# Performance work log

Hardware: AMD Instinct MI355X
Metric: run time of the kernel (lower is better)

Reference implementation:

```python
import jax, jax.numpy as jnp
import numpy as np

NG, ND, NS, E, DIM, H = 20000, 8000, 8000, 300000, 256, 8
HD = DIM // H
SCALE = 1.0 / float(np.sqrt(HD))
EPS = 1e-5


def _ln(x, g, b):
    mu = x.mean(-1, keepdims=True)
    var = ((x - mu) ** 2).mean(-1, keepdims=True)
    return (x - mu) / jnp.sqrt(var + EPS) * g + b


def _attn(h_src, h_dst, Wq, bq, Wk, bk, Wv, bv, src, dst, n_dst):
    # multi-head edge dot-product attention with edge_softmax over incoming edges
    Q = (h_dst @ Wq.T + bq).reshape(-1, H, HD)
    K = (h_src @ Wk.T + bk).reshape(-1, H, HD)
    V = (h_src @ Wv.T + bv).reshape(-1, H, HD)
    score = jnp.einsum('ehd,ehd->eh', K[src], Q[dst]) * SCALE  # [E, H]
    m = jax.ops.segment_max(score, dst, num_segments=n_dst)
    m = jnp.where(jnp.isfinite(m), m, 0.0)  # nodes with no in-edges
    a = jnp.exp(score - m[dst])
    denom = jax.ops.segment_sum(a, dst, num_segments=n_dst)
    a = a / denom[dst]
    h = jax.ops.segment_sum(V[src] * a[:, :, None], dst, num_segments=n_dst)
    return h.reshape(n_dst, DIM)


def _bahdanau(m1, m2, W1, b1, W2, b2, v, bv):
    e1 = (jnp.tanh(m1 @ W1.T + b1) @ v.T + bv)[:, 0]
    e2 = (jnp.tanh(m2 @ W2.T + b2) @ v.T + bv)[:, 0]
    w = jax.nn.softmax(jnp.stack([e1, e2], axis=1), axis=1)
    return w[:, 0:1] * m1 + w[:, 1:2] * m2


def _forward(gene_feat, drug_feat, disease_feat,
             dg_Wq, dg_bq, dg_Wk, dg_bk, dg_Wv, dg_bv,
             disg_Wq, disg_bq, disg_Wk, disg_bk, disg_Wv, disg_bv,
             gd_Wq, gd_bq, gd_Wk, gd_bk, gd_Wv, gd_bv,
             gdis_Wq, gdis_bq, gdis_Wk, gdis_bk, gdis_Wv, gdis_bv,
             f_W1, f_b1, f_W2, f_b2, f_v, f_bv,
             ln1_g, ln1_b, ln2_g, ln2_b,
             dg_src, dg_dst, disg_src, disg_dst, gd_src, gd_dst, gdis_src, gdis_dst):
    gm_drug = _attn(drug_feat, gene_feat, dg_Wq, dg_bq, dg_Wk, dg_bk, dg_Wv, dg_bv, dg_src, dg_dst, NG)
    gm_dis = _attn(disease_feat, gene_feat, disg_Wq, disg_bq, disg_Wk, disg_bk, disg_Wv, disg_bv, disg_src, disg_dst, NG)
    has_d = jnp.zeros((NG,), bool).at[dg_dst].set(True)
    has_s = jnp.zeros((NG,), bool).at[disg_dst].set(True)
    fused = _bahdanau(gm_drug, gm_dis, f_W1, f_b1, f_W2, f_b2, f_v, f_bv)
    gene_msg = jnp.where((has_d & has_s)[:, None], fused,
                         jnp.where(has_d[:, None], gm_drug,
                                   jnp.where(has_s[:, None], gm_dis, 0.0)))
    gene_out = _ln(gene_feat + jax.nn.gelu(gene_msg, approximate=False), ln1_g, ln1_b)
    drug_msg = _attn(gene_out, drug_feat, gd_Wq, gd_bq, gd_Wk, gd_bk, gd_Wv, gd_bv, gd_src, gd_dst, ND)
    dis_msg = _attn(gene_out, disease_feat, gdis_Wq, gdis_bq, gdis_Wk, gdis_bk, gdis_Wv, gdis_bv, gdis_src, gdis_dst, NS)
    drug_out = _ln(drug_feat + jax.nn.gelu(drug_msg, approximate=False), ln2_g, ln2_b)
    disease_out = _ln(disease_feat + jax.nn.gelu(dis_msg, approximate=False), ln2_g, ln2_b)
    return (drug_out, disease_out, gene_out)


def setup_inputs() -> dict:
    ks = jax.random.split(jax.random.key(0), 40)
    it = iter(range(40))

    def nrm(shape):
        return jax.random.normal(ks[next(it)], shape, dtype=jnp.float32)

    def xav(din, dout):
        lim = float(np.sqrt(6.0 / (din + dout)))
        return jax.random.uniform(ks[next(it)], (dout, din), minval=-lim, maxval=lim, dtype=jnp.float32)

    def ridx(n, hi):
        return jax.random.randint(ks[next(it)], (n,), 0, hi, dtype=jnp.int32)

    inp = {}
    inp['gene_feat'] = nrm((NG, DIM))
    inp['drug_feat'] = nrm((ND, DIM))
    inp['disease_feat'] = nrm((NS, DIM))
    for p in ['dg', 'disg', 'gd', 'gdis']:
        inp[p + '_Wq'] = xav(DIM, DIM)
        inp[p + '_bq'] = jnp.zeros((DIM,), jnp.float32)
        inp[p + '_Wk'] = xav(DIM, DIM)
        inp[p + '_bk'] = jnp.zeros((DIM,), jnp.float32)
        inp[p + '_Wv'] = xav(DIM, DIM)
        inp[p + '_bv'] = jnp.zeros((DIM,), jnp.float32)
    inp['f_W1'] = xav(DIM, DIM); inp['f_b1'] = jnp.zeros((DIM,), jnp.float32)
    inp['f_W2'] = xav(DIM, DIM); inp['f_b2'] = jnp.zeros((DIM,), jnp.float32)
    inp['f_v'] = xav(DIM, 1); inp['f_bv'] = jnp.zeros((1,), jnp.float32)
    inp['ln1_g'] = jnp.ones((DIM,), jnp.float32); inp['ln1_b'] = jnp.zeros((DIM,), jnp.float32)
    inp['ln2_g'] = jnp.ones((DIM,), jnp.float32); inp['ln2_b'] = jnp.zeros((DIM,), jnp.float32)
    inp['dg_src'] = ridx(E, ND); inp['dg_dst'] = ridx(E, NG)
    inp['disg_src'] = ridx(E, NS); inp['disg_dst'] = ridx(E, NG)
    inp['gd_src'] = ridx(E, NG); inp['gd_dst'] = ridx(E, ND)
    inp['gdis_src'] = ridx(E, NG); inp['gdis_dst'] = ridx(E, NS)
    return inp


def reference(gene_feat, drug_feat, disease_feat,
              dg_Wq, dg_bq, dg_Wk, dg_bk, dg_Wv, dg_bv,
              disg_Wq, disg_bq, disg_Wk, disg_bk, disg_Wv, disg_bv,
              gd_Wq, gd_bq, gd_Wk, gd_bk, gd_Wv, gd_bv,
              gdis_Wq, gdis_bq, gdis_Wk, gdis_bk, gdis_Wv, gdis_bv,
              f_W1, f_b1, f_W2, f_b2, f_v, f_bv,
              ln1_g, ln1_b, ln2_g, ln2_b,
              dg_src, dg_dst, disg_src, disg_dst, gd_src, gd_dst, gdis_src, gdis_dst):
    return _forward(gene_feat, drug_feat, disease_feat,
                    dg_Wq, dg_bq, dg_Wk, dg_bk, dg_Wv, dg_bv,
                    disg_Wq, disg_bq, disg_Wk, disg_bk, disg_Wv, disg_bv,
                    gd_Wq, gd_bq, gd_Wk, gd_bk, gd_Wv, gd_bv,
                    gdis_Wq, gdis_bq, gdis_Wk, gdis_bk, gdis_Wv, gdis_bv,
                    f_W1, f_b1, f_W2, f_b2, f_v, f_bv,
                    ln1_g, ln1_b, ln2_g, ln2_b,
                    dg_src, dg_dst, disg_src, disg_dst, gd_src, gd_dst, gdis_src, gdis_dst)
```

## Files before the change

### kernel.cpp

```cpp
#include <hip/hip_runtime.h>

#define NG 20000
#define ND 8000
#define NS 8000
#define EE 300000
#define DIM 256
#define SCALE_QK 0.17677669529663687f
#define LNEPS 1e-5f

#define MAXB 40
#define L1CH 2048
#define NCH1 ((EE + L1CH - 1) / L1CH)
#define CB_G 8704
#define CB_S 10496
#define RB_G (40 * CB_G)
#define RB_S (32 * CB_S)

typedef __attribute__((ext_vector_type(4))) float floatx4;
typedef __attribute__((ext_vector_type(8))) short shortx8;
typedef __attribute__((ext_vector_type(8))) unsigned short ushortx8;
typedef unsigned int u32;

__device__ __forceinline__ float bf2f(unsigned short u) {
    union { unsigned u; float f; } c; c.u = ((unsigned)u) << 16; return c.f;
}
__device__ __forceinline__ unsigned short f2bf(float f) {
    union { float f; unsigned u; } c; c.f = f;
    return (unsigned short)((c.u + 0x7fffu + ((c.u >> 16) & 1u)) >> 16);
}
__device__ __forceinline__ float gelu_exact(float v) {
    return 0.5f * v * (1.0f + erff(v * 0.70710678118654752f));
}

__device__ __forceinline__ void async_load16(const unsigned short* g,
                                             unsigned short* lds) {
    __builtin_amdgcn_global_load_lds(
        (const __attribute__((address_space(1))) u32*)(const void*)g,
        (__attribute__((address_space(3))) u32*)(void*)lds, 16, 0, 0);
}

__device__ __forceinline__ int swzoff(int row, int q) {
    int p = (row >> 1) & 7, b = row & 1;
    return ((row >> 4) * 64 + p * 8 + (((b << 2) + q) ^ p)) * 8;
}

template <int MODE, int KVI>
__global__ __launch_bounds__(256, 4) void gemm_nt(
    const unsigned short* __restrict__ A, const unsigned short* __restrict__ W,
    const float* __restrict__ bias1, const float* __restrict__ bias2,
    const float* __restrict__ bias3, const float* __restrict__ bias4,
    unsigned short* __restrict__ C, int ldc,
    const float* __restrict__ vvec, float* __restrict__ evec, int M)
{
    __shared__ unsigned short As[2][128 * 32];
    __shared__ unsigned short Bs[2][64 * 32];
    const int tid = threadIdx.x;
    const int lane = tid & 63, wv = tid >> 6;
    const int quad = lane >> 4, l16 = lane & 15;
    const int m0 = blockIdx.x * 128;
    const int n0 = blockIdx.y * 64;

    const int sp = lane >> 3, ss = lane & 7;
    const int srow = 2 * sp + ((ss ^ sp) >> 2);
    const int sq = (ss ^ sp) & 3;
    const unsigned short* gA0 = A + (size_t)(m0 + wv * 16 + srow) * 256 + sq * 8;
    const unsigned short* gA1 = A + (size_t)(m0 + 64 + wv * 16 + srow) * 256 + sq * 8;
    const unsigned short* gB  = W + (size_t)(n0 + wv * 16 + srow) * 256 + sq * 8;

    floatx4 acc[2][4];
#pragma unroll
    for (int i = 0; i < 2; ++i)
#pragma unroll
        for (int j = 0; j < 4; ++j) acc[i][j] = (floatx4){0.f, 0.f, 0.f, 0.f};

    async_load16(gA0, &As[0][(wv * 16) * 32]);
    async_load16(gA1, &As[0][(64 + wv * 16) * 32]);
    async_load16(gB,  &Bs[0][(wv * 16) * 32]);
    __syncthreads();

    for (int k0 = 0; k0 < 256; k0 += 32) {
        const int buf = (k0 >> 5) & 1;
        if (k0 < 224) {
            const int nb = buf ^ 1;
            async_load16(gA0 + k0 + 32, &As[nb][(wv * 16) * 32]);
            async_load16(gA1 + k0 + 32, &As[nb][(64 + wv * 16) * 32]);
            async_load16(gB + k0 + 32,  &Bs[nb][(wv * 16) * 32]);
        }
        shortx8 af[2], bfr[4];
#pragma unroll
        for (int mf = 0; mf < 2; ++mf)
            af[mf] = *(const shortx8*)(&As[buf][swzoff(wv * 32 + mf * 16 + l16, quad)]);
#pragma unroll
        for (int nf = 0; nf < 4; ++nf)
            bfr[nf] = *(const shortx8*)(&Bs[buf][swzoff(nf * 16 + l16, quad)]);
#pragma unroll
        for (int mf = 0; mf < 2; ++mf)
#pragma unroll
            for (int nf = 0; nf < 4; ++nf)
                acc[mf][nf] = __builtin_amdgcn_mfma_f32_16x16x32_bf16(
                    af[mf], bfr[nf], acc[mf][nf], 0, 0, 0);
        __syncthreads();
    }

    if (MODE == 0) {
#pragma unroll
        for (int mf = 0; mf < 2; ++mf)
#pragma unroll
            for (int r = 0; r < 4; ++r) {
                int m = m0 + wv * 32 + mf * 16 + quad * 4 + r;
                if (m < M) {
#pragma unroll
                    for (int nf = 0; nf < 4; ++nf) {
                        int n = n0 + nf * 16 + l16;
                        int h = n >> 8;
                        const float* bp = (h == 0) ? bias1 : (h == 1) ? bias2
                                        : (h == 2) ? bias3 : bias4;
                        float bn = bp[n & 255];
                        int pos;
                        if (KVI) {
                            int nn = n & 511;
                            pos = (n & ~511) + ((nn & 255) >> 2) * 8 + (nn & 3) +
                                  ((nn >> 8) << 2);
                        } else {
                            pos = n;
                        }
                        C[(size_t)m * ldc + pos] = f2bf(acc[mf][nf][r] + bn);
                    }
                }
            }
    } else {
        float p[2][4] = {};
#pragma unroll
        for (int mf = 0; mf < 2; ++mf)
#pragma unroll
            for (int nf = 0; nf < 4; ++nf) {
                int n = n0 + nf * 16 + l16;
                float vn = vvec[n];
                float bn = bias1[n];
#pragma unroll
                for (int r = 0; r < 4; ++r)
                    p[mf][r] += vn * tanhf(acc[mf][nf][r] + bn);
            }
#pragma unroll
        for (int mf = 0; mf < 2; ++mf)
#pragma unroll
            for (int r = 0; r < 4; ++r) {
                float s = p[mf][r];
                s += __shfl_xor(s, 1); s += __shfl_xor(s, 2);
                s += __shfl_xor(s, 4); s += __shfl_xor(s, 8);
                if (l16 == 0) {
                    int m = m0 + wv * 32 + mf * 16 + quad * 4 + r;
                    if (m < M) atomicAdd(&evec[m], s);
                }
            }
    }
}

struct PrepP {
    int* zb; int zn; int nzb;
    const float* wsrc[14];
    unsigned short* wout;
    const float* gf; const float* df; const float* sf;
    unsigned short* go; unsigned short* dfo; unsigned short* so;
};
__global__ void prep_kernel(PrepP p) {
    int bid = blockIdx.x, tid = threadIdx.x;
    if (bid < p.nzb) {
        int i = bid * 256 + tid;
        if (i < p.zn) p.zb[i] = 0;
        return;
    }
    bid -= p.nzb;
    if (bid < 896) {
        int idx = bid * 256 + tid;
        int mat = idx >> 14;
        int e = (idx & 16383) << 2;
        float4 f = *(const float4*)(p.wsrc[mat] + e);
        ushort4 t;
        t.x = f2bf(f.x); t.y = f2bf(f.y); t.z = f2bf(f.z); t.w = f2bf(f.w);
        *(ushort4*)(p.wout + ((size_t)mat << 16) + e) = t;
        return;
    }
    bid -= 896;
    const int NG4 = NG * 64, ND4 = ND * 64, NS4 = NS * 64;
    int i = bid * 256 + tid;
    const float* in; unsigned short* out; int j;
    if (i < NG4) { in = p.gf; out = p.go; j = i; }
    else if (i < NG4 + ND4) { in = p.df; out = p.dfo; j = i - NG4; }
    else if (i < NG4 + ND4 + NS4) { in = p.sf; out = p.so; j = i - NG4 - ND4; }
    else return;
    float4 f = *(const float4*)(in + (size_t)j * 4);
    ushort4 t;
    t.x = f2bf(f.x); t.y = f2bf(f.y); t.z = f2bf(f.z); t.w = f2bf(f.w);
    *(ushort4*)(out + (size_t)j * 4) = t;
}

__global__ void fillf_kernel(float* __restrict__ p, int n, float v) {
    int i = blockIdx.x * blockDim.x + threadIdx.x;
    if (i < n) p[i] = v;
}

struct L1P {
    const int* src[4];
    const int* dst[4];
    int* brec[4];
    int* bcur;
};
__global__ __launch_bounds__(256) void l1_bucket_kernel(L1P a) {
    __shared__ int hist[MAXB];
    int g = blockIdx.x / NCH1, c = blockIdx.x - g * NCH1;
    int base = c * L1CH;
    int tid = threadIdx.x;
    const int shift = (g < 2) ? 9 : 8;
    const int CB = (g < 2) ? CB_G : CB_S;
    const int NB = (g < 2) ? 40 : 32;
    if (tid < NB) hist[tid] = 0;
    __syncthreads();
    const int* __restrict__ dstp = a.dst[g];
    const int* __restrict__ srcp = a.src[g];
    int bk[8], rec[8], lr[8];
#pragma unroll
    for (int j = 0; j < 8; ++j) {
        int e = base + j * 256 + tid;
        bool ok = e < EE;
        int dd = ok ? dstp[e] : 0;
        int ss = ok ? srcp[e] : 0;
        bk[j] = dd >> shift;
        rec[j] = ((dd & ((1 << shift) - 1)) << 15) | ss;
        lr[j] = ok ? atomicAdd(&hist[bk[j]], 1) : -1;
    }
    __syncthreads();
    if (tid < NB) {
        int h = hist[tid];
        if (h > 0) hist[tid] = atomicAdd(&a.bcur[g * MAXB + tid], h);
    }
    __syncthreads();
    int* __restrict__ recp = a.brec[g];
#pragma unroll
    for (int j = 0; j < 8; ++j) {
        if (lr[j] >= 0) {
            int pos = hist[bk[j]] + lr[j];
            if (pos < CB) recp[bk[j] * CB + pos] = rec[j];
        }
    }
}

struct L2P {
    const int* brec[4];
    const int* bcur;
    int* cnt[4];
    int* offs[4];
    int* srcs[4];
};
__global__ __launch_bounds__(256) void l2_csr_kernel(L2P a) {
    __shared__ int hist[512];
    __shared__ int loffs[512];
    __shared__ int cur[512];
    __shared__ int ws2[4];
    __shared__ int bb;
    int bid = blockIdx.x, tid = threadIdx.x;
    int g, b;
    if (bid < 40) { g = 0; b = bid; }
    else if (bid < 80) { g = 1; b = bid - 40; }
    else if (bid < 112) { g = 2; b = bid - 80; }
    else { g = 3; b = bid - 112; }
    const int shift = (g < 2) ? 9 : 8;
    const int BSZ = 1 << shift;
    const int CB = (g < 2) ? CB_G : CB_S;
    const int N = (g < 2) ? NG : ((g == 2) ? ND : NS);
    hist[tid] = 0; hist[256 + tid] = 0;
    if (tid == 0) {
        int s = 0;
        const int* bc = a.bcur + g * MAXB;
        for (int i = 0; i < b; ++i) s += bc[i];
        bb = s;
    }
    __syncthreads();
    int total = a.bcur[g * MAXB + b];
    if (total > CB) total = CB;
    const int* __restrict__ recp = a.brec[g] + b * CB;
    for (int i = tid; i < total; i += 256)
        atomicAdd(&hist[recp[i] >> 15], 1);
    __syncthreads();
    int v0 = hist[2 * tid], v1 = hist[2 * tid + 1];
    int s = v0 + v1, x = s;
    int lane = tid & 63, wv = tid >> 6;
#pragma unroll
    for (int o = 1; o < 64; o <<= 1) {
        int u = __shfl_up(x, o);
        if (lane >= o) x += u;
    }
    if (lane == 63) ws2[wv] = x;
    __syncthreads();
    int woff = 0;
    for (int w = 0; w < wv; ++w) woff += ws2[w];
    int excl = woff + x - s;
    loffs[2 * tid] = excl; loffs[2 * tid + 1] = excl + v0;
    cur[2 * tid] = excl;  cur[2 * tid + 1] = excl + v0;
    int base = bb;
    int lo = b << shift;
    for (int i = tid; i < BSZ; i += 256) {
        int d = lo + i;
        if (d < N) {
            a.cnt[g][d] = hist[i];
            a.offs[g][d] = base + loffs[i];
        }
    }
    __syncthreads();
    int* __restrict__ sp = a.srcs[g];
    for (int i = tid; i < total; i += 256) {
        int rec = recp[i];
        int pos = atomicAdd(&cur[rec >> 15], 1);
        sp[base + pos] = rec & 0x7fff;
    }
}

__device__ __forceinline__ void wave_attn_node(
    const unsigned short* __restrict__ Q, int qs,
    const unsigned short* __restrict__ KV,
    const int* __restrict__ offs, const int* __restrict__ cnt,
    const int* __restrict__ srcs, int du, int lane,
    float& g0, float& g1, float& g2, float& g3)
{
    const int lo = lane * 4;
    const int lofs = lane * 8;
    ushort4 qv = *(const ushort4*)(Q + (size_t)du * qs + lo);
    const float q0 = bf2f(qv.x), q1 = bf2f(qv.y), q2 = bf2f(qv.z), q3 = bf2f(qv.w);
    const int beg = offs[du], num = cnt[du];

    float m[8], l[8], a[8][4];
#pragma unroll
    for (int c = 0; c < 8; ++c) {
        m[c] = -INFINITY; l[c] = 0.f;
        a[c][0] = a[c][1] = a[c][2] = a[c][3] = 0.f;
    }

    for (int i = 0; i < num; i += 8) {
        ushortx8 kv[8];
#pragma unroll
        for (int c = 0; c < 8; ++c) {
            int idx = i + c;
            int cidx = (idx < num) ? idx : (num - 1);
            int s = srcs[beg + cidx];
            kv[c] = *(const ushortx8*)(KV + (size_t)s * 512 + lofs);
        }
        float p[8];
#pragma unroll
        for (int c = 0; c < 8; ++c)
            p[c] = q0 * bf2f(kv[c][0]) + q1 * bf2f(kv[c][1]) +
                   q2 * bf2f(kv[c][2]) + q3 * bf2f(kv[c][3]);
#pragma unroll
        for (int c = 0; c < 8; ++c) p[c] += __shfl_xor(p[c], 1);
#pragma unroll
        for (int c = 0; c < 8; ++c) p[c] += __shfl_xor(p[c], 2);
#pragma unroll
        for (int c = 0; c < 8; ++c) p[c] += __shfl_xor(p[c], 4);
#pragma unroll
        for (int c = 0; c < 8; ++c) {
            if (i + c < num) {
                float sc = p[c] * SCALE_QK;
                float mn = fmaxf(m[c], sc);
                float eo = __expf(m[c] - mn);
                float en = __expf(sc - mn);
                a[c][0] = a[c][0] * eo + en * bf2f(kv[c][4]);
                a[c][1] = a[c][1] * eo + en * bf2f(kv[c][5]);
                a[c][2] = a[c][2] * eo + en * bf2f(kv[c][6]);
                a[c][3] = a[c][3] * eo + en * bf2f(kv[c][7]);
                l[c] = l[c] * eo + en;
                m[c] = mn;
            }
        }
    }

    float ms = fmaxf(fmaxf(fmaxf(m[0], m[1]), fmaxf(m[2], m[3])),
                     fmaxf(fmaxf(m[4], m[5]), fmaxf(m[6], m[7])));
    float A0 = 0.f, A1 = 0.f, A2 = 0.f, A3 = 0.f, L = 0.f;
    if (ms > -INFINITY) {
#pragma unroll
        for (int c = 0; c < 8; ++c) {
            float w = __expf(m[c] - ms);
            A0 += a[c][0] * w; A1 += a[c][1] * w;
            A2 += a[c][2] * w; A3 += a[c][3] * w;
            L += l[c] * w;
        }
    }
    float inv = (L > 0.f) ? 1.f / L : 0.f;
    g0 = A0 * inv; g1 = A1 * inv; g2 = A2 * inv; g3 = A3 * inv;
}

__device__ __forceinline__ void wave_ln_store(
    float x0, float x1, float x2, float x3,
    const float* __restrict__ g, const float* __restrict__ b,
    float* __restrict__ out, unsigned short* __restrict__ out_bf,
    int du, int lo)
{
    float s1 = x0 + x1 + x2 + x3;
    float s2 = x0 * x0 + x1 * x1 + x2 * x2 + x3 * x3;
#pragma unroll
    for (int o = 1; o < 64; o <<= 1) {
        s1 += __shfl_xor(s1, o);
        s2 += __shfl_xor(s2, o);
    }
    float mu = s1 * (1.f / 256.f);
    float var = fmaxf(s2 * (1.f / 256.f) - mu * mu, 0.f);
    float rs = rsqrtf(var + LNEPS);
    float4 gv = *(const float4*)(g + lo);
    float4 bv = *(const float4*)(b + lo);
    float y0 = (x0 - mu) * rs * gv.x + bv.x;
    float y1 = (x1 - mu) * rs * gv.y + bv.y;
    float y2 = (x2 - mu) * rs * gv.z + bv.z;
    float y3 = (x3 - mu) * rs * gv.w + bv.w;
    *(float4*)(out + (size_t)du * 256 + lo) = make_float4(y0, y1, y2, y3);
    if (out_bf) {
        ushort4 t; t.x = f2bf(y0); t.y = f2bf(y1); t.z = f2bf(y2); t.w = f2bf(y3);
        *(ushort4*)(out_bf + (size_t)du * 256 + lo) = t;
    }
}

__global__ __launch_bounds__(256) void agg_gm_kernel(
    const unsigned short* __restrict__ Q, int qs,
    const unsigned short* __restrict__ KV,
    const int* __restrict__ offs, const int* __restrict__ cnt,
    const int* __restrict__ srcs, unsigned short* __restrict__ gm, int N)
{
    int lane = threadIdx.x & 63, wv = threadIdx.x >> 6;
    int d = blockIdx.x * 4 + wv;
    if (d >= N) return;
    int du = __builtin_amdgcn_readfirstlane(d);
    float g0, g1, g2, g3;
    wave_attn_node(Q, qs, KV, offs, cnt, srcs, du, lane, g0, g1, g2, g3);
    ushort4 t; t.x = f2bf(g0); t.y = f2bf(g1); t.z = f2bf(g2); t.w = f2bf(g3);
    *(ushort4*)(gm + (size_t)du * 256 + lane * 4) = t;
}

__global__ __launch_bounds__(256) void agg_ln_kernel(
    const unsigned short* __restrict__ Q, int qs,
    const unsigned short* __restrict__ KV,
    const int* __restrict__ offs, const int* __restrict__ cnt,
    const int* __restrict__ srcs, const float* __restrict__ feat,
    const float* __restrict__ g, const float* __restrict__ b,
    float* __restrict__ out, int N)
{
    int lane = threadIdx.x & 63, wv = threadIdx.x >> 6;
    int d = blockIdx.x * 4 + wv;
    if (d >= N) return;
    int du = __builtin_amdgcn_readfirstlane(d);
    int lo = lane * 4;
    float g0, g1, g2, g3;
    wave_attn_node(Q, qs, KV, offs, cnt, srcs, du, lane, g0, g1, g2, g3);
    float4 fv = *(const float4*)(feat + (size_t)du * 256 + lo);
    float x0 = fv.x + gelu_exact(g0);
    float x1 = fv.y + gelu_exact(g1);
    float x2 = fv.z + gelu_exact(g2);
    float x3 = fv.w + gelu_exact(g3);
    wave_ln_store(x0, x1, x2, x3, g, b, out, nullptr, du, lo);
}

__global__ __launch_bounds__(256) void gene_fusion_kernel(
    const float* __restrict__ gene_feat, const unsigned short* __restrict__ gm_d,
    const unsigned short* __restrict__ gm_s, const float* __restrict__ e1,
    const float* __restrict__ e2, const int* __restrict__ cnt_d,
    const int* __restrict__ cnt_s, const float* __restrict__ g,
    const float* __restrict__ b, float* __restrict__ out,
    unsigned short* __restrict__ out_bf)
{
    int lane = threadIdx.x & 63, wv = threadIdx.x >> 6;
    int d = blockIdx.x * 4 + wv;
    if (d >= NG) return;
    int du = __builtin_amdgcn_readfirstlane(d);
    int lo = lane * 4;
    ushort4 v1 = *(const ushort4*)(gm_d + (size_t)du * 256 + lo);
    ushort4 v2 = *(const ushort4*)(gm_s + (size_t)du * 256 + lo);
    bool hd = cnt_d[du] > 0, hs = cnt_s[du] > 0;
    float wa, wb;
    if (hd && hs) {
        float aa = e1[du], bb = e2[du];
        float mm = fmaxf(aa, bb);
        float ea = __expf(aa - mm), eb = __expf(bb - mm);
        float inv = 1.f / (ea + eb);
        wa = ea * inv; wb = eb * inv;
    } else if (hd) { wa = 1.f; wb = 0.f; }
    else if (hs) { wa = 0.f; wb = 1.f; }
    else { wa = 0.f; wb = 0.f; }
    float m0 = wa * bf2f(v1.x) + wb * bf2f(v2.x);
    float m1 = wa * bf2f(v1.y) + wb * bf2f(v2.y);
    float m2 = wa * bf2f(v1.z) + wb * bf2f(v2.z);
    float m3 = wa * bf2f(v1.w) + wb * bf2f(v2.w);
    float4 fv = *(const float4*)(gene_feat + (size_t)du * 256 + lo);
    float x0 = fv.x + gelu_exact(m0);
    float x1 = fv.y + gelu_exact(m1);
    float x2 = fv.z + gelu_exact(m2);
    float x3 = fv.w + gelu_exact(m3);
    wave_ln_store(x0, x1, x2, x3, g, b, out, out_bf, du, lo);
}

extern "C" void kernel_launch(void* const* d_in, const int* in_sizes, int n_in,
                              void* d_out, int out_size, void* d_ws, size_t ws_size,
                              hipStream_t stream)
{
    float* out_f32 = (float*)d_out;

    const float* gene_feat    = (const float*)d_in[0];
    const float* drug_feat    = (const float*)d_in[1];
    const float* disease_feat = (const float*)d_in[2];
    const float* dg_Wq = (const float*)d_in[3];
    const float* dg_bq = (const float*)d_in[4];
    const float* dg_Wk = (const float*)d_in[5];
    const float* dg_bk = (const float*)d_in[6];
    const float* dg_Wv = (const float*)d_in[7];
    const float* dg_bv = (const float*)d_in[8];
    const float* disg_Wq = (const float*)d_in[9];
    const float* disg_bq = (const float*)d_in[10];
    const float* disg_Wk = (const float*)d_in[11];
    const float* disg_bk = (const float*)d_in[12];
    const float* disg_Wv = (const float*)d_in[13];
    const float* disg_bv = (const float*)d_in[14];
    const float* gd_Wq = (const float*)d_in[15];
    const float* gd_bq = (const float*)d_in[16];
    const float* gd_Wk = (const float*)d_in[17];
    const float* gd_bk = (const float*)d_in[18];
    const float* gd_Wv = (const float*)d_in[19];
    const float* gd_bv = (const float*)d_in[20];
    const float* gdis_Wq = (const float*)d_in[21];
    const float* gdis_bq = (const float*)d_in[22];
    const float* gdis_Wk = (const float*)d_in[23];
    const float* gdis_bk = (const float*)d_in[24];
    const float* gdis_Wv = (const float*)d_in[25];
    const float* gdis_bv = (const float*)d_in[26];
    const float* f_W1 = (const float*)d_in[27];
    const float* f_b1 = (const float*)d_in[28];
    const float* f_W2 = (const float*)d_in[29];
    const float* f_b2 = (const float*)d_in[30];
    const float* f_v  = (const float*)d_in[31];
    const float* ln1_g = (const float*)d_in[33];
    const float* ln1_b = (const float*)d_in[34];
    const float* ln2_g = (const float*)d_in[35];
    const float* ln2_b = (const float*)d_in[36];
    const int* dg_src   = (const int*)d_in[37];
    const int* dg_dst   = (const int*)d_in[38];
    const int* disg_src = (const int*)d_in[39];
    const int* disg_dst = (const int*)d_in[40];
    const int* gd_src   = (const int*)d_in[41];
    const int* gd_dst   = (const int*)d_in[42];
    const int* gdis_src = (const int*)d_in[43];
    const int* gdis_dst = (const int*)d_in[44];

    char* ws = (char*)d_ws;
    size_t off = 0;
    auto alloc = [&](size_t bytes) -> char* {
        char* p = ws + off;
        off += (bytes + 511) & ~(size_t)511;
        return p;
    };
    int* bcur = (int*)alloc(4 * MAXB * 4);
    float* e1 = (float*)alloc(NG * 4);
    float* e2 = (float*)alloc(NG * 4);
    size_t zero_len = off;
    int* offs_dg   = (int*)alloc(NG * 4);
    int* offs_disg = (int*)alloc(NG * 4);
    int* offs_gd   = (int*)alloc(ND * 4);
    int* offs_gdis = (int*)alloc(NS * 4);
    int* cnt_dg    = (int*)alloc(NG * 4);
    int* cnt_disg  = (int*)alloc(NG * 4);
    int* cnt_gd    = (int*)alloc(ND * 4);
    int* cnt_gdis  = (int*)alloc(NS * 4);
    int* srcs_dg   = (int*)alloc((size_t)EE * 4);
    int* srcs_disg = (int*)alloc((size_t)EE * 4);
    int* srcs_gd   = (int*)alloc((size_t)EE * 4);
    int* srcs_gdis = (int*)alloc((size_t)EE * 4);
    unsigned short* Q12  = (unsigned short*)alloc((size_t)NG * 512 * 2);
    unsigned short* KVb  = (unsigned short*)alloc((size_t)NG * 512 * 2);
    unsigned short* gm_d = (unsigned short*)alloc((size_t)NG * 256 * 2);
    unsigned short* gm_s = (unsigned short*)alloc((size_t)NG * 256 * 2);
    unsigned short* gene_bf = (unsigned short*)alloc((size_t)NG * 256 * 2);
    unsigned short* drug_bf = (unsigned short*)alloc((size_t)ND * 256 * 2);
    unsigned short* dis_bf  = (unsigned short*)alloc((size_t)NS * 256 * 2);
    unsigned short* Wbf     = (unsigned short*)alloc((size_t)14 * 65536 * 2);
    char* guard = alloc(64 * 1024);
    (void)guard;
    size_t need = off;

    int* brec0 = (int*)Q12;
    int* brec1 = brec0 + RB_G;
    int* brec2 = brec1 + RB_G;
    int* brec3 = brec2 + RB_S;

    unsigned short* gene_out_bf = gm_d;

    float* out_drug = out_f32;
    float* out_dis  = out_drug + (size_t)ND * 256;
    float* out_gene = out_dis + (size_t)NS * 256;

    if (ws_size < need) {
        fillf_kernel<<<(out_size + 255) / 256, 256, 0, stream>>>(out_f32, out_size, 1000.0f);
        return;
    }

    {
        PrepP p;
        p.zb = (int*)d_ws;
        p.zn = (int)(zero_len / 4);
        p.nzb = (p.zn + 255) / 256;
        const float* wl[14] = {dg_Wq, disg_Wq, dg_Wk, dg_Wv, disg_Wk, disg_Wv,
                               gd_Wk, gd_Wv, gdis_Wk, gdis_Wv, gd_Wq, gdis_Wq,
                               f_W1, f_W2};
        for (int i = 0; i < 14; ++i) p.wsrc[i] = wl[i];
        p.wout = Wbf;
        p.gf = gene_feat; p.df = drug_feat; p.sf = disease_feat;
        p.go = gene_bf; p.dfo = drug_bf; p.so = dis_bf;
        int nfeat = ((NG + ND + NS) * 64 + 255) / 256;
        prep_kernel<<<p.nzb + 896 + nfeat, 256, 0, stream>>>(p);
    }

    {
        L1P p;
        p.src[0] = dg_src; p.src[1] = disg_src; p.src[2] = gd_src; p.src[3] = gdis_src;
        p.dst[0] = dg_dst; p.dst[1] = disg_dst; p.dst[2] = gd_dst; p.dst[3] = gdis_dst;
        p.brec[0] = brec0; p.brec[1] = brec1; p.brec[2] = brec2; p.brec[3] = brec3;
        p.bcur = bcur;
        l1_bucket_kernel<<<4 * NCH1, 256, 0, stream>>>(p);
    }
    {
        L2P p;
        p.brec[0] = brec0; p.brec[1] = brec1; p.brec[2] = brec2; p.brec[3] = brec3;
        p.bcur = bcur;
        p.cnt[0] = cnt_dg; p.cnt[1] = cnt_disg; p.cnt[2] = cnt_gd; p.cnt[3] = cnt_gdis;
        p.offs[0] = offs_dg; p.offs[1] = offs_disg; p.offs[2] = offs_gd; p.offs[3] = offs_gdis;
        p.srcs[0] = srcs_dg; p.srcs[1] = srcs_disg; p.srcs[2] = srcs_gd; p.srcs[3] = srcs_gdis;
        l2_csr_kernel<<<144, 256, 0, stream>>>(p);
    }

    {
        dim3 gq((NG + 127) / 128, 8);
        gemm_nt<0, 0><<<gq, 256, 0, stream>>>(gene_bf, Wbf, dg_bq, disg_bq,
                                              dg_bq, dg_bq, Q12, 512,
                                              nullptr, nullptr, NG);
    }
    {
        dim3 gkv((ND + 127) / 128, 8);
        gemm_nt<0, 1><<<gkv, 256, 0, stream>>>(drug_bf, Wbf + (size_t)2 * 65536,
                                               dg_bk, dg_bv, dg_bk, dg_bk,
                                               KVb, 512, nullptr, nullptr, ND);
    }
    agg_gm_kernel<<<(NG + 3) / 4, 256, 0, stream>>>(Q12, 512, KVb, offs_dg, cnt_dg,
                                                    srcs_dg, gm_d, NG);
    {
        dim3 gkv((NS + 127) / 128, 8);
        gemm_nt<0, 1><<<gkv, 256, 0, stream>>>(dis_bf, Wbf + (size_t)4 * 65536,
                                               disg_bk, disg_bv, disg_bk, disg_bk,
                                               KVb, 512, nullptr, nullptr, NS);
    }
    agg_gm_kernel<<<(NG + 3) / 4, 256, 0, stream>>>(Q12 + 256, 512, KVb, offs_disg,
                                                    cnt_disg, srcs_disg, gm_s, NG);

    {
        dim3 gb((NG + 127) / 128, 4);
        gemm_nt<1, 0><<<gb, 256, 0, stream>>>(gm_d, Wbf + (size_t)12 * 65536,
                                              f_b1, f_b1, f_b1, f_b1,
                                              nullptr, 256, f_v, e1, NG);
        gemm_nt<1, 0><<<gb, 256, 0, stream>>>(gm_s, Wbf + (size_t)13 * 65536,
                                              f_b2, f_b2, f_b2, f_b2,
                                              nullptr, 256, f_v, e2, NG);
    }
    gene_fusion_kernel<<<(NG + 3) / 4, 256, 0, stream>>>(
        gene_feat, gm_d, gm_s, e1, e2, cnt_dg, cnt_disg, ln1_g, ln1_b,
        out_gene, gene_out_bf);

    {
        dim3 gq((ND + 127) / 128, 4);
        gemm_nt<0, 0><<<gq, 256, 0, stream>>>(drug_bf, Wbf + (size_t)10 * 65536,
                                              gd_bq, gd_bq, gd_bq, gd_bq,
                                              Q12, 256, nullptr, nullptr, ND);
    }
    {
        dim3 gkv((NG + 127) / 128, 8);
        gemm_nt<0, 1><<<gkv, 256, 0, stream>>>(gene_out_bf, Wbf + (size_t)6 * 65536,
                                               gd_bk, gd_bv, gd_bk, gd_bk,
                                               KVb, 512, nullptr, nullptr, NG);
    }
    agg_ln_kernel<<<(ND + 3) / 4, 256, 0, stream>>>(Q12, 256, KVb, offs_gd, cnt_gd,
                                                    srcs_gd, drug_feat, ln2_g, ln2_b,
                                                    out_drug, ND);

    {
        dim3 gq((NS + 127) / 128, 4);
        gemm_nt<0, 0><<<gq, 256, 0, stream>>>(dis_bf, Wbf + (size_t)11 * 65536,
                                              gdis_bq, gdis_bq, gdis_bq, gdis_bq,
                                              Q12, 256, nullptr, nullptr, NS);
    }
    {
        dim3 gkv((NG + 127) / 128, 8);
        gemm_nt<0, 1><<<gkv, 256, 0, stream>>>(gene_out_bf, Wbf + (size_t)8 * 65536,
                                               gdis_bk, gdis_bv, gdis_bk, gdis_bk,
                                               KVb, 512, nullptr, nullptr, NG);
    }
    agg_ln_kernel<<<(NS + 3) / 4, 256, 0, stream>>>(Q12, 256, KVb, offs_gdis, cnt_gdis,
                                                    srcs_gdis, disease_feat, ln2_g, ln2_b,
                                                    out_dis, NS);
}
```

Baseline: 515.9 us.

## Batch independent GEMMs and attention aggregations into fewer launches, prefetch edge sources

Replaces the templated GEMM with a descriptor-driven batch kernel, so independent projections (Q, drug/disease KV, Bahdanau scores, reverse Q, both reverse KV) share one launch through blockIdx.z. The two gene aggregations and the two LN aggregations are likewise merged into single launches. Buffers are remapped (KVs1b, KVb2 alias gm_s, Qd/Qs) so the batched outputs do not overwrite one another. The aggregation loop also software-prefetches the next 8 source indices to hide index-load latency. The goal is fewer small launches and better GPU fill; the cost is runtime mode branches in place of template specialisation, wasted early-exit blocks in the padded grids, and aliasing risk.

```diff
diff --git a/kernel.cpp b/kernel.cpp
--- a/kernel.cpp
+++ b/kernel.cpp
@@ -44,28 +44,35 @@
     return ((row >> 4) * 64 + p * 8 + (((b << 2) + q) ^ p)) * 8;
 }
 
-template <int MODE, int KVI>
-__global__ __launch_bounds__(256, 4) void gemm_nt(
-    const unsigned short* __restrict__ A, const unsigned short* __restrict__ W,
-    const float* __restrict__ bias1, const float* __restrict__ bias2,
-    const float* __restrict__ bias3, const float* __restrict__ bias4,
-    unsigned short* __restrict__ C, int ldc,
-    const float* __restrict__ vvec, float* __restrict__ evec, int M)
+struct GemmDesc {
+    const unsigned short* A; const unsigned short* W;
+    const float* b1; const float* b2; const float* b3; const float* b4;
+    unsigned short* C; int ldc;
+    const float* vvec; float* evec;
+    int M; int gx; int ncol; int mode; int kvi;
+};
+struct GemmBatch { GemmDesc d[4]; };
+
+__global__ __launch_bounds__(256, 4) void gemm_batch_kernel(GemmBatch gb)
 {
     __shared__ unsigned short As[2][128 * 32];
     __shared__ unsigned short Bs[2][64 * 32];
+    const GemmDesc d = gb.d[blockIdx.z];
+    if ((int)blockIdx.x >= d.gx) return;
+    const int n0 = blockIdx.y * 64;
+    if (n0 >= d.ncol) return;
+
     const int tid = threadIdx.x;
     const int lane = tid & 63, wv = tid >> 6;
     const int quad = lane >> 4, l16 = lane & 15;
     const int m0 = blockIdx.x * 128;
-    const int n0 = blockIdx.y * 64;
 
     const int sp = lane >> 3, ss = lane & 7;
     const int srow = 2 * sp + ((ss ^ sp) >> 2);
     const int sq = (ss ^ sp) & 3;
-    const unsigned short* gA0 = A + (size_t)(m0 + wv * 16 + srow) * 256 + sq * 8;
-    const unsigned short* gA1 = A + (size_t)(m0 + 64 + wv * 16 + srow) * 256 + sq * 8;
-    const unsigned short* gB  = W + (size_t)(n0 + wv * 16 + srow) * 256 + sq * 8;
+    const unsigned short* gA0 = d.A + (size_t)(m0 + wv * 16 + srow) * 256 + sq * 8;
+    const unsigned short* gA1 = d.A + (size_t)(m0 + 64 + wv * 16 + srow) * 256 + sq * 8;
+    const unsigned short* gB  = d.W + (size_t)(n0 + wv * 16 + srow) * 256 + sq * 8;
 
     floatx4 acc[2][4];
 #pragma unroll
@@ -102,29 +109,29 @@
         __syncthreads();
     }
 
-    if (MODE == 0) {
+    if (d.mode == 0) {
 #pragma unroll
         for (int mf = 0; mf < 2; ++mf)
 #pragma unroll
             for (int r = 0; r < 4; ++r) {
                 int m = m0 + wv * 32 + mf * 16 + quad * 4 + r;
-                if (m < M) {
+                if (m < d.M) {
 #pragma unroll
                     for (int nf = 0; nf < 4; ++nf) {
                         int n = n0 + nf * 16 + l16;
                         int h = n >> 8;
-                        const float* bp = (h == 0) ? bias1 : (h == 1) ? bias2
-                                        : (h == 2) ? bias3 : bias4;
+                        const float* bp = (h == 0) ? d.b1 : (h == 1) ? d.b2
+                                        : (h == 2) ? d.b3 : d.b4;
                         float bn = bp[n & 255];
                         int pos;
-                        if (KVI) {
+                        if (d.kvi) {
                             int nn = n & 511;
                             pos = (n & ~511) + ((nn & 255) >> 2) * 8 + (nn & 3) +
                                   ((nn >> 8) << 2);
                         } else {
                             pos = n;
                         }
-                        C[(size_t)m * ldc + pos] = f2bf(acc[mf][nf][r] + bn);
+                        d.C[(size_t)m * d.ldc + pos] = f2bf(acc[mf][nf][r] + bn);
                     }
                 }
             }
@@ -135,8 +142,8 @@
 #pragma unroll
             for (int nf = 0; nf < 4; ++nf) {
                 int n = n0 + nf * 16 + l16;
-                float vn = vvec[n];
-                float bn = bias1[n];
+                float vn = d.vvec[n];
+                float bn = d.b1[n];
 #pragma unroll
                 for (int r = 0; r < 4; ++r)
                     p[mf][r] += vn * tanhf(acc[mf][nf][r] + bn);
@@ -150,7 +157,7 @@
                 s += __shfl_xor(s, 4); s += __shfl_xor(s, 8);
                 if (l16 == 0) {
                     int m = m0 + wv * 32 + mf * 16 + quad * 4 + r;
-                    if (m < M) atomicAdd(&evec[m], s);
+                    if (m < d.M) atomicAdd(&d.evec[m], s);
                 }
             }
     }
@@ -300,10 +307,10 @@
     int base = bb;
     int lo = b << shift;
     for (int i = tid; i < BSZ; i += 256) {
-        int d = lo + i;
-        if (d < N) {
-            a.cnt[g][d] = hist[i];
-            a.offs[g][d] = base + loffs[i];
+        int dd = lo + i;
+        if (dd < N) {
+            a.cnt[g][dd] = hist[i];
+            a.offs[g][dd] = base + loffs[i];
         }
     }
     __syncthreads();
@@ -335,15 +342,27 @@
         a[c][0] = a[c][1] = a[c][2] = a[c][3] = 0.f;
     }
 
+    int sb[8];
+    if (num > 0) {
+#pragma unroll
+        for (int c = 0; c < 8; ++c)
+            sb[c] = srcs[beg + ((c < num) ? c : (num - 1))];
+    }
+
     for (int i = 0; i < num; i += 8) {
+        int sn[8];
+        const bool more = (i + 8) < num;
+        if (more) {
+#pragma unroll
+            for (int c = 0; c < 8; ++c) {
+                int idx = i + 8 + c;
+                sn[c] = srcs[beg + ((idx < num) ? idx : (num - 1))];
+            }
+        }
         ushortx8 kv[8];
 #pragma unroll
-        for (int c = 0; c < 8; ++c) {
-            int idx = i + c;
-            int cidx = (idx < num) ? idx : (num - 1);
-            int s = srcs[beg + cidx];
-            kv[c] = *(const ushortx8*)(KV + (size_t)s * 512 + lofs);
-        }
+        for (int c = 0; c < 8; ++c)
+            kv[c] = *(const ushortx8*)(KV + (size_t)sb[c] * 512 + lofs);
         float p[8];
 #pragma unroll
         for (int c = 0; c < 8; ++c)
@@ -370,6 +389,10 @@
                 m[c] = mn;
             }
         }
+        if (more) {
+#pragma unroll
+            for (int c = 0; c < 8; ++c) sb[c] = sn[c];
+        }
     }
 
     float ms = fmaxf(fmaxf(fmaxf(m[0], m[1]), fmaxf(m[2], m[3])),
@@ -417,43 +440,38 @@
     }
 }
 
-__global__ __launch_bounds__(256) void agg_gm_kernel(
-    const unsigned short* __restrict__ Q, int qs,
-    const unsigned short* __restrict__ KV,
-    const int* __restrict__ offs, const int* __restrict__ cnt,
-    const int* __restrict__ srcs, unsigned short* __restrict__ gm, int N)
+struct AggDesc {
+    const unsigned short* Q; int qs;
+    const unsigned short* KV;
+    const int* offs; const int* cnt; const int* srcs;
+    unsigned short* gm;
+    const float* feat; const float* g; const float* b; float* out;
+    int N;
+};
+template <int LN>
+__global__ __launch_bounds__(256) void agg2_kernel(AggDesc a0, AggDesc a1, int nb0)
 {
+    const bool first = (int)blockIdx.x < nb0;
+    const AggDesc d = first ? a0 : a1;
+    const int bx = first ? blockIdx.x : (blockIdx.x - nb0);
     int lane = threadIdx.x & 63, wv = threadIdx.x >> 6;
-    int d = blockIdx.x * 4 + wv;
-    if (d >= N) return;
-    int du = __builtin_amdgcn_readfirstlane(d);
-    float g0, g1, g2, g3;
-    wave_attn_node(Q, qs, KV, offs, cnt, srcs, du, lane, g0, g1, g2, g3);
-    ushort4 t; t.x = f2bf(g0); t.y = f2bf(g1); t.z = f2bf(g2); t.w = f2bf(g3);
-    *(ushort4*)(gm + (size_t)du * 256 + lane * 4) = t;
-}
-
-__global__ __launch_bounds__(256) void agg_ln_kernel(
-    const unsigned short* __restrict__ Q, int qs,
-    const unsigned short* __restrict__ KV,
-    const int* __restrict__ offs, const int* __restrict__ cnt,
-    const int* __restrict__ srcs, const float* __restrict__ feat,
-    const float* __restrict__ g, const float* __restrict__ b,
-    float* __restrict__ out, int N)
-{
-    int lane = threadIdx.x & 63, wv = threadIdx.x >> 6;
-    int d = blockIdx.x * 4 + wv;
-    if (d >= N) return;
-    int du = __builtin_amdgcn_readfirstlane(d);
+    int nd = bx * 4 + wv;
+    if (nd >= d.N) return;
+    int du = __builtin_amdgcn_readfirstlane(nd);
     int lo = lane * 4;
     float g0, g1, g2, g3;
-    wave_attn_node(Q, qs, KV, offs, cnt, srcs, du, lane, g0, g1, g2, g3);
-    float4 fv = *(const float4*)(feat + (size_t)du * 256 + lo);
-    float x0 = fv.x + gelu_exact(g0);
-    float x1 = fv.y + gelu_exact(g1);
-    float x2 = fv.z + gelu_exact(g2);
-    float x3 = fv.w + gelu_exact(g3);
-    wave_ln_store(x0, x1, x2, x3, g, b, out, nullptr, du, lo);
+    wave_attn_node(d.Q, d.qs, d.KV, d.offs, d.cnt, d.srcs, du, lane, g0, g1, g2, g3);
+    if (LN == 0) {
+        ushort4 t; t.x = f2bf(g0); t.y = f2bf(g1); t.z = f2bf(g2); t.w = f2bf(g3);
+        *(ushort4*)(d.gm + (size_t)du * 256 + lo) = t;
+    } else {
+        float4 fv = *(const float4*)(d.feat + (size_t)du * 256 + lo);
+        float x0 = fv.x + gelu_exact(g0);
+        float x1 = fv.y + gelu_exact(g1);
+        float x2 = fv.z + gelu_exact(g2);
+        float x3 = fv.w + gelu_exact(g3);
+        wave_ln_store(x0, x1, x2, x3, d.g, d.b, d.out, nullptr, du, lo);
+    }
 }
 
 __global__ __launch_bounds__(256) void gene_fusion_kernel(
@@ -585,6 +603,10 @@
     int* brec2 = brec1 + RB_G;
     int* brec3 = brec2 + RB_S;
 
+    unsigned short* KVb2 = gm_s;
+    unsigned short* KVs1b = KVb + (size_t)ND * 512;
+    unsigned short* Qd = Q12;
+    unsigned short* Qs = Q12 + (size_t)ND * 256;
     unsigned short* gene_out_bf = gm_d;
 
     float* out_drug = out_f32;
@@ -630,71 +652,84 @@
         l2_csr_kernel<<<144, 256, 0, stream>>>(p);
     }
 
+    const int GXG = (NG + 127) / 128;
+    const int GXS = (ND + 127) / 128;
+
+    auto mkd = [](const unsigned short* A, const unsigned short* W,
+                  const float* b1, const float* b2, const float* b3, const float* b4,
+                  unsigned short* C, int ldc, const float* vv, float* ev,
+                  int M, int gx, int ncol, int mode, int kvi) {
+        GemmDesc d;
+        d.A = A; d.W = W; d.b1 = b1; d.b2 = b2; d.b3 = b3; d.b4 = b4;
+        d.C = C; d.ldc = ldc; d.vvec = vv; d.evec = ev;
+        d.M = M; d.gx = gx; d.ncol = ncol; d.mode = mode; d.kvi = kvi;
+        return d;
+    };
+    auto mka = [](const unsigned short* Q, int qs, const unsigned short* KV,
+                  const int* offs, const int* cnt, const int* srcs,
+                  unsigned short* gm, const float* feat, const float* g,
+                  const float* b, float* out, int N) {
+        AggDesc d;
+        d.Q = Q; d.qs = qs; d.KV = KV; d.offs = offs; d.cnt = cnt; d.srcs = srcs;
+        d.gm = gm; d.feat = feat; d.g = g; d.b = b; d.out = out; d.N = N;
+        return d;
+    };
+
     {
-        dim3 gq((NG + 127) / 128, 8);
-        gemm_nt<0, 0><<<gq, 256, 0, stream>>>(gene_bf, Wbf, dg_bq, disg_bq,
-                                              dg_bq, dg_bq, Q12, 512,
-                                              nullptr, nullptr, NG);
-    }
+        GemmBatch gb;
+        gb.d[0] = mkd(gene_bf, Wbf, dg_bq, disg_bq, dg_bq, dg_bq,
+                      Q12, 512, nullptr, nullptr, NG, GXG, 512, 0, 0);
+        gb.d[1] = mkd(drug_bf, Wbf + (size_t)2 * 65536, dg_bk, dg_bv, dg_bk, dg_bk,
+                      KVb, 512, nullptr, nullptr, ND, GXS, 512, 0, 1);
+        gb.d[2] = mkd(dis_bf, Wbf + (size_t)4 * 65536, disg_bk, disg_bv, disg_bk, disg_bk,
+                      KVs1b, 512, nullptr, nullptr, NS, GXS, 512, 0, 1);
+        gb.d[3] = gb.d[2]; gb.d[3].gx = 0;
+        gemm_batch_kernel<<<dim3(GXG, 8, 3), 256, 0, stream>>>(gb);
+    }
+
     {
-        dim3 gkv((ND + 127) / 128, 8);
-        gemm_nt<0, 1><<<gkv, 256, 0, stream>>>(drug_bf, Wbf + (size_t)2 * 65536,
-                                               dg_bk, dg_bv, dg_bk, dg_bk,
-                                               KVb, 512, nullptr, nullptr, ND);
-    }
-    agg_gm_kernel<<<(NG + 3) / 4, 256, 0, stream>>>(Q12, 512, KVb, offs_dg, cnt_dg,
-                                                    srcs_dg, gm_d, NG);
+        AggDesc a0 = mka(Q12, 512, KVb, offs_dg, cnt_dg, srcs_dg,
+                         gm_d, nullptr, nullptr, nullptr, nullptr, NG);
+        AggDesc a1 = mka(Q12 + 256, 512, KVs1b, offs_disg, cnt_disg, srcs_disg,
+                         gm_s, nullptr, nullptr, nullptr, nullptr, NG);
+        int nb = (NG + 3) / 4;
+        agg2_kernel<0><<<2 * nb, 256, 0, stream>>>(a0, a1, nb);
+    }
+
     {
-        dim3 gkv((NS + 127) / 128, 8);
-        gemm_nt<0, 1><<<gkv, 256, 0, stream>>>(dis_bf, Wbf + (size_t)4 * 65536,
-                                               disg_bk, disg_bv, disg_bk, disg_bk,
-                                               KVb, 512, nullptr, nullptr, NS);
-    }
-    agg_gm_kernel<<<(NG + 3) / 4, 256, 0, stream>>>(Q12 + 256, 512, KVb, offs_disg,
-                                                    cnt_disg, srcs_disg, gm_s, NG);
-
-    {
-        dim3 gb((NG + 127) / 128, 4);
-        gemm_nt<1, 0><<<gb, 256, 0, stream>>>(gm_d, Wbf + (size_t)12 * 65536,
-                                              f_b1, f_b1, f_b1, f_b1,
-                                              nullptr, 256, f_v, e1, NG);
-        gemm_nt<1, 0><<<gb, 256, 0, stream>>>(gm_s, Wbf + (size_t)13 * 65536,
-                                              f_b2, f_b2, f_b2, f_b2,
-                                              nullptr, 256, f_v, e2, NG);
-    }
+        GemmBatch gb;
+        gb.d[0] = mkd(gm_d, Wbf + (size_t)12 * 65536, f_b1, f_b1, f_b1, f_b1,
+                      nullptr, 256, f_v, e1, NG, GXG, 256, 1, 0);
+        gb.d[1] = mkd(gm_s, Wbf + (size_t)13 * 65536, f_b2, f_b2, f_b2, f_b2,
+                      nullptr, 256, f_v, e2, NG, GXG, 256, 1, 0);
+        gb.d[2] = mkd(drug_bf, Wbf + (size_t)10 * 65536, gd_bq, gd_bq, gd_bq, gd_bq,
+                      Qd, 256, nullptr, nullptr, ND, GXS, 256, 0, 0);
+        gb.d[3] = mkd(dis_bf, Wbf + (size_t)11 * 65536, gdis_bq, gdis_bq, gdis_bq, gdis_bq,
+                      Qs, 256, nullptr, nullptr, NS, GXS, 256, 0, 0);
+        gemm_batch_kernel<<<dim3(GXG, 4, 4), 256, 0, stream>>>(gb);
+    }
+
     gene_fusion_kernel<<<(NG + 3) / 4, 256, 0, stream>>>(
         gene_feat, gm_d, gm_s, e1, e2, cnt_dg, cnt_disg, ln1_g, ln1_b,
         out_gene, gene_out_bf);
 
     {
-        dim3 gq((ND + 127) / 128, 4);
-        gemm_nt<0, 0><<<gq, 256, 0, stream>>>(drug_bf, Wbf + (size_t)10 * 65536,
-                                              gd_bq, gd_bq, gd_bq, gd_bq,
-                                              Q12, 256, nullptr, nullptr, ND);
-    }
+        GemmBatch gb;
+        gb.d[0] = mkd(gene_out_bf, Wbf + (size_t)6 * 65536, gd_bk, gd_bv, gd_bk, gd_bk,
+                      KVb, 512, nullptr, nullptr, NG, GXG, 512, 0, 1);
+        gb.d[1] = mkd(gene_out_bf, Wbf + (size_t)8 * 65536, gdis_bk, gdis_bv, gdis_bk, gdis_bk,
+                      KVb2, 512, nullptr, nullptr, NG, GXG, 512, 0, 1);
+        gb.d[2] = gb.d[1]; gb.d[2].gx = 0;
+        gb.d[3] = gb.d[1]; gb.d[3].gx = 0;
+        gemm_batch_kernel<<<dim3(GXG, 8, 2), 256, 0, stream>>>(gb);
+    }
+
     {
-        dim3 gkv((NG + 127) / 128, 8);
-        gemm_nt<0, 1><<<gkv, 256, 0, stream>>>(gene_out_bf, Wbf + (size_t)6 * 65536,
-                                               gd_bk, gd_bv, gd_bk, gd_bk,
-                                               KVb, 512, nullptr, nullptr, NG);
-    }
-    agg_ln_kernel<<<(ND + 3) / 4, 256, 0, stream>>>(Q12, 256, KVb, offs_gd, cnt_gd,
-                                                    srcs_gd, drug_feat, ln2_g, ln2_b,
-                                                    out_drug, ND);
-
-    {
-        dim3 gq((NS + 127) / 128, 4);
-        gemm_nt<0, 0><<<gq, 256, 0, stream>>>(dis_bf, Wbf + (size_t)11 * 65536,
-                                              gdis_bq, gdis_bq, gdis_bq, gdis_bq,
-                                              Q12, 256, nullptr, nullptr, NS);
-    }
-    {
-        dim3 gkv((NG + 127) / 128, 8);
-        gemm_nt<0, 1><<<gkv, 256, 0, stream>>>(gene_out_bf, Wbf + (size_t)8 * 65536,
-                                               gdis_bk, gdis_bv, gdis_bk, gdis_bk,
-                                               KVb, 512, nullptr, nullptr, NG);
-    }
-    agg_ln_kernel<<<(NS + 3) / 4, 256, 0, stream>>>(Q12, 256, KVb, offs_gdis, cnt_gdis,
-                                                    srcs_gdis, disease_feat, ln2_g, ln2_b,
-                                                    out_dis, NS);
-}
+        AggDesc a0 = mka(Qd, 256, KVb, offs_gd, cnt_gd, srcs_gd,
+                         nullptr, drug_feat, ln2_g, ln2_b, out_drug, ND);
+        AggDesc a1 = mka(Qs, 256, KVb2, offs_gdis, cnt_gdis, srcs_gdis,
+                         nullptr, disease_feat, ln2_g, ln2_b, out_dis, NS);
+        int nb = (ND + 3) / 4;
+        agg2_kernel<1><<<2 * nb, 256, 0, stream>>>(a0, a1, nb);
+    }
+}
```

Measured after the change: 485.0 us. -6.0%, faster.
